# Kernel tuning notes

Hardware: AMD Instinct MI355X
Metric: run time of the kernel (lower is better)

The kernel has to match this reference:

```python
import jax, jax.numpy as jnp
import numpy as np

TEMPERATURE = 1.0
EPS = 1e-5
COS_EPS = 1e-8  # torch CosineSimilarity default eps
N_POS, N_NEG, D = 512, 512, 512


def setup_inputs() -> dict:
    key = jax.random.key(0)
    k1, k2, k3 = jax.random.split(key, 3)
    tensor_positive = jax.random.normal(k1, (N_POS, D), dtype=jnp.float32)
    tensor_negative = jax.random.normal(k2, (N_NEG, D), dtype=jnp.float32)
    # nn.Linear(512*3, 1), weight ~ N(0, 0.02^2), bias zeros
    linear_w = jax.random.normal(k3, (1, 3 * D), dtype=jnp.float32) * 0.02
    linear_b = jnp.zeros((1,), dtype=jnp.float32)
    return {"tensor_positive": tensor_positive, "tensor_negative": tensor_negative,
            "linear_w": linear_w, "linear_b": linear_b}


def _cos_matrix(a, b):
    # pairwise cosine similarity [Na, Nb], matching torch CosineSimilarity eps clamp
    an = a / jnp.maximum(jnp.linalg.norm(a, axis=-1, keepdims=True), COS_EPS)
    bn = b / jnp.maximum(jnp.linalg.norm(b, axis=-1, keepdims=True), COS_EPS)
    return an @ bn.T


def reference(tensor_positive, tensor_negative, linear_w, linear_b):
    pos, neg = tensor_positive, tensor_negative
    n_pos, d = pos.shape
    n_neg = neg.shape[0]

    # NCE part
    logit_n = jnp.exp(_cos_matrix(pos, neg) / TEMPERATURE)        # [N, M]
    deno_n = jnp.sum(logit_n, axis=-1)                            # [N]
    logit_p = jnp.exp(_cos_matrix(pos, pos) / TEMPERATURE)        # [N, N]
    loss = jnp.sum(-jnp.log(logit_p / (deno_n[:, None] + logit_p + EPS)))

    # Pairwise classifier: linear(cat([a, b, |a-b|])) decomposed as
    # a@w1 + b@w2 + |a-b|@w3 to avoid materializing the 3D concat.
    w = linear_w[0]
    w1, w2, w3 = w[:d], w[d:2 * d], w[2 * d:]
    allv = jnp.concatenate([pos, neg], axis=0)                    # [N+M, D]
    t1 = pos @ w1                                                 # [N]
    t2 = allv @ w2                                                # [N+M]
    diff = jnp.abs(pos[:, None, :] - allv[None, :, :])            # [N, N+M, D]
    t3 = jnp.einsum('nmd,d->nm', diff, w3)                        # [N, N+M]
    logits = t1[:, None] + t2[None, :] + t3 + linear_b[0]
    labels = jnp.concatenate([jnp.ones((n_pos,), jnp.float32),
                              jnp.zeros((n_neg,), jnp.float32)])  # [N+M]
    # BCE(sigmoid(logits), labels), stable form; per-i mean then sum over i
    bce = labels[None, :] * jax.nn.softplus(-logits) + (1.0 - labels[None, :]) * jax.nn.softplus(logits)
    loss = loss + jnp.sum(jnp.mean(bce, axis=1))
    return loss
```

## Files before the change

kernel.cpp:

```cpp
#include <hip/hip_runtime.h>
#include <math.h>

#define NPOS 512
#define DIM  512
#define NB   1024
#define EPSV 1e-5f
#define COS_EPS 1e-8f
#define ZSPLIT 4
#define KSLICE (DIM / ZSPLIT)

#define OFF_INV 0
#define OFF_T1  1024
#define OFF_T2  1536
#define OFF_P   2560
#define OFF_Q   (OFF_P + ZSPLIT * NPOS * NB)

__device__ __forceinline__ float softplus_f(float x) {
    return fmaxf(x, 0.f) + __logf(1.f + __expf(-fabsf(x)));
}

__global__ __launch_bounds__(256) void prep_kernel(
    const float* __restrict__ pos, const float* __restrict__ neg,
    const float* __restrict__ w, float* __restrict__ ws, float* __restrict__ out)
{
    int gtid = blockIdx.x * 256 + threadIdx.x;
    if (gtid == 0) out[0] = 0.f;
    int row  = gtid >> 6;
    int lane = threadIdx.x & 63;
    if (row >= NB) return;
    bool is_pos = row < NPOS;
    const float* r = is_pos ? pos + row * DIM : neg + (row - NPOS) * DIM;

    const float4* r4  = (const float4*)r + lane * 2;
    const float4* w14 = (const float4*)(w) + lane * 2;
    const float4* w24 = (const float4*)(w + DIM) + lane * 2;
    float4 a0 = r4[0],  a1 = r4[1];
    float4 u0 = w14[0], u1 = w14[1];
    float4 v0 = w24[0], v1 = w24[1];

    float ss  = a0.x*a0.x + a0.y*a0.y + a0.z*a0.z + a0.w*a0.w
              + a1.x*a1.x + a1.y*a1.y + a1.z*a1.z + a1.w*a1.w;
    float dw1 = a0.x*u0.x + a0.y*u0.y + a0.z*u0.z + a0.w*u0.w
              + a1.x*u1.x + a1.y*u1.y + a1.z*u1.z + a1.w*u1.w;
    float dw2 = a0.x*v0.x + a0.y*v0.y + a0.z*v0.z + a0.w*v0.w
              + a1.x*v1.x + a1.y*v1.y + a1.z*v1.z + a1.w*v1.w;

    #pragma unroll
    for (int off = 32; off; off >>= 1) {
        ss  += __shfl_xor(ss, off);
        dw1 += __shfl_xor(dw1, off);
        dw2 += __shfl_xor(dw2, off);
    }
    if (lane == 0) {
        float inv = 1.f / fmaxf(sqrtf(ss), COS_EPS);
        ws[OFF_INV + row] = inv;
        ws[OFF_T2 + row]  = dw2;
        if (is_pos) ws[OFF_T1 + row] = dw1;
    }
}

__global__ __launch_bounds__(256) void fused_kernel(
    const float* __restrict__ pos, const float* __restrict__ neg,
    const float* __restrict__ w, float* __restrict__ ws)
{
    __shared__ __align__(16) float As[64][36];
    __shared__ __align__(16) float Bs[64][36];

    const int tid = threadIdx.x;
    const int n0 = blockIdx.y * 64;
    const int m0 = blockIdx.x * 64;
    const int z  = blockIdx.z;
    const float* Asrc = pos + (size_t)n0 * DIM + z * KSLICE;
    const float* Bsrc = ((m0 < NPOS) ? (pos + (size_t)m0 * DIM)
                                     : (neg + (size_t)(m0 - NPOS) * DIM)) + z * KSLICE;
    const float* w3 = w + 2 * DIM + z * KSLICE;

    const int lr = tid >> 3;
    const int lc = (tid & 7) << 2;
    const int ti = tid >> 4;
    const int tj = tid & 15;

    float c[4][4] = {{0.f}}, t[4][4] = {{0.f}};

    float4 a0 = *(const float4*)(Asrc + lr * DIM + lc);
    float4 a1 = *(const float4*)(Asrc + (lr + 32) * DIM + lc);
    float4 b0 = *(const float4*)(Bsrc + lr * DIM + lc);
    float4 b1 = *(const float4*)(Bsrc + (lr + 32) * DIM + lc);
    *(float4*)&As[lr][lc]      = a0;
    *(float4*)&As[lr + 32][lc] = a1;
    *(float4*)&Bs[lr][lc]      = b0;
    *(float4*)&Bs[lr + 32][lc] = b1;
    __syncthreads();

    #pragma unroll 1
    for (int iter = 0; iter < KSLICE / 32; ++iter) {
        const bool more = (iter < KSLICE / 32 - 1);
        if (more) {
            const float* ap = Asrc + (iter + 1) * 32;
            const float* bp = Bsrc + (iter + 1) * 32;
            a0 = *(const float4*)(ap + lr * DIM + lc);
            a1 = *(const float4*)(ap + (lr + 32) * DIM + lc);
            b0 = *(const float4*)(bp + lr * DIM + lc);
            b1 = *(const float4*)(bp + (lr + 32) * DIM + lc);
        }
        const float* w3i = w3 + iter * 32;
        #pragma unroll
        for (int k = 0; k < 32; k += 4) {
            float4 av[4], bv[4];
            #pragma unroll
            for (int r = 0; r < 4; ++r) av[r] = *(const float4*)&As[ti + 16 * r][k];
            #pragma unroll
            for (int s = 0; s < 4; ++s) bv[s] = *(const float4*)&Bs[tj + 16 * s][k];
            const float4 wv = *(const float4*)(w3i + k);
            #pragma unroll
            for (int r = 0; r < 4; ++r) {
                #pragma unroll
                for (int s = 0; s < 4; ++s) {
                    c[r][s] = fmaf(av[r].x, bv[s].x, c[r][s]);
                    c[r][s] = fmaf(av[r].y, bv[s].y, c[r][s]);
                    c[r][s] = fmaf(av[r].z, bv[s].z, c[r][s]);
                    c[r][s] = fmaf(av[r].w, bv[s].w, c[r][s]);
                    t[r][s] = fmaf(fabsf(av[r].x - bv[s].x), wv.x, t[r][s]);
                    t[r][s] = fmaf(fabsf(av[r].y - bv[s].y), wv.y, t[r][s]);
                    t[r][s] = fmaf(fabsf(av[r].z - bv[s].z), wv.z, t[r][s]);
                    t[r][s] = fmaf(fabsf(av[r].w - bv[s].w), wv.w, t[r][s]);
                }
            }
        }
        if (more) {
            __syncthreads();
            *(float4*)&As[lr][lc]      = a0;
            *(float4*)&As[lr + 32][lc] = a1;
            *(float4*)&Bs[lr][lc]      = b0;
            *(float4*)&Bs[lr + 32][lc] = b1;
            __syncthreads();
        }
    }

    float* Sp = ws + OFF_P + (size_t)z * NPOS * NB;
    float* Tp = ws + OFF_Q + (size_t)z * NPOS * NB;
    #pragma unroll
    for (int r = 0; r < 4; ++r) {
        int n = n0 + ti + 16 * r;
        #pragma unroll
        for (int s = 0; s < 4; ++s) {
            int m = m0 + tj + 16 * s;
            Sp[(size_t)n * NB + m] = c[r][s];
            Tp[(size_t)n * NB + m] = t[r][s];
        }
    }
}

__global__ __launch_bounds__(128) void finish_kernel(
    const float* __restrict__ lb, float* __restrict__ ws, float* __restrict__ out)
{
    const int n = blockIdx.x * 2 + (threadIdx.x >> 6);
    const int l = threadIdx.x & 63;
    const float4* S[ZSPLIT];
    const float4* T[ZSPLIT];
    #pragma unroll
    for (int zz = 0; zz < ZSPLIT; ++zz) {
        S[zz] = (const float4*)(ws + OFF_P + (size_t)zz * NPOS * NB + (size_t)n * NB);
        T[zz] = (const float4*)(ws + OFF_Q + (size_t)zz * NPOS * NB + (size_t)n * NB);
    }
    const float invn = ws[OFF_INV + n];
    const float t1n  = ws[OFF_T1 + n];
    const float bias = lb[0];

    float4 cj[4];
    float eneg = 0.f;
    #pragma unroll
    for (int j = 0; j < 4; ++j) {
        int i4 = l + 64 * j;
        float4 s0 = S[0][i4], s1 = S[1][i4], s2 = S[2][i4], s3 = S[3][i4];
        float4 inv4 = *(const float4*)(ws + OFF_INV + 4 * i4);
        float4 cc;
        cc.x = (s0.x + s1.x + s2.x + s3.x) * invn * inv4.x;
        cc.y = (s0.y + s1.y + s2.y + s3.y) * invn * inv4.y;
        cc.z = (s0.z + s1.z + s2.z + s3.z) * invn * inv4.z;
        cc.w = (s0.w + s1.w + s2.w + s3.w) * invn * inv4.w;
        cj[j] = cc;
        if (j >= 2)
            eneg += __expf(cc.x) + __expf(cc.y) + __expf(cc.z) + __expf(cc.w);
    }
    #pragma unroll
    for (int off = 32; off; off >>= 1) eneg += __shfl_xor(eneg, off);

    float part = 0.f;
    #pragma unroll
    for (int j = 0; j < 2; ++j) {
        float4 cc = cj[j];
        part += __logf(eneg + __expf(cc.x) + EPSV) - cc.x;
        part += __logf(eneg + __expf(cc.y) + EPSV) - cc.y;
        part += __logf(eneg + __expf(cc.z) + EPSV) - cc.z;
        part += __logf(eneg + __expf(cc.w) + EPSV) - cc.w;
    }

    float bce = 0.f;
    #pragma unroll
    for (int j = 0; j < 4; ++j) {
        int i4 = l + 64 * j;
        float4 t0 = T[0][i4], t1 = T[1][i4], t2_ = T[2][i4], t3_ = T[3][i4];
        float4 tw = *(const float4*)(ws + OFF_T2 + 4 * i4);
        float4 lg;
        lg.x = t1n + tw.x + t0.x + t1.x + t2_.x + t3_.x + bias;
        lg.y = t1n + tw.y + t0.y + t1.y + t2_.y + t3_.y + bias;
        lg.z = t1n + tw.z + t0.z + t1.z + t2_.z + t3_.z + bias;
        lg.w = t1n + tw.w + t0.w + t1.w + t2_.w + t3_.w + bias;
        if (j < 2)
            bce += softplus_f(-lg.x) + softplus_f(-lg.y) + softplus_f(-lg.z) + softplus_f(-lg.w);
        else
            bce += softplus_f(lg.x) + softplus_f(lg.y) + softplus_f(lg.z) + softplus_f(lg.w);
    }
    part += bce * (1.f / 1024.f);

    #pragma unroll
    for (int off = 32; off; off >>= 1) part += __shfl_xor(part, off);
    if (l == 0) atomicAdd(out, part);
}

extern "C" void kernel_launch(void* const* d_in, const int* in_sizes, int n_in,
                              void* d_out, int out_size, void* d_ws, size_t ws_size,
                              hipStream_t stream) {
    (void)in_sizes; (void)n_in; (void)out_size; (void)ws_size;
    const float* pos = (const float*)d_in[0];
    const float* neg = (const float*)d_in[1];
    const float* w   = (const float*)d_in[2];
    const float* lb  = (const float*)d_in[3];
    float* out = (float*)d_out;
    float* ws  = (float*)d_ws;

    prep_kernel<<<256, 256, 0, stream>>>(pos, neg, w, ws, out);
    fused_kernel<<<dim3(16, 8, ZSPLIT), 256, 0, stream>>>(pos, neg, w, ws);
    finish_kernel<<<256, 128, 0, stream>>>(lb, ws, out);
}
```

Measured before the change: 109.9 us.

## Drop split-K partials and fuse BCE and negative row sums into main kernel epilogue

Removes the 4-way K split that wrote large partial S and T matrices to workspace. The fused kernel now loops over the full D dimension with 32x64 output tiles. Its epilogue computes the BCE softplus terms and the exp row sums over negatives directly, accumulating them with atomics. Only the positive-positive cosine block is stored for the finish kernel. This cuts tens of MB of workspace writes and reads. The cost is a longer per-block K loop, 256 blocks instead of 512, and per-element atomics for the denominators and the output.

Result: no change. 108.6 us (-1.1%).

```diff
diff --git a/kernel.cpp b/kernel.cpp
--- a/kernel.cpp
+++ b/kernel.cpp
@@ -6,14 +6,12 @@
 #define NB   1024
 #define EPSV 1e-5f
 #define COS_EPS 1e-8f
-#define ZSPLIT 4
-#define KSLICE (DIM / ZSPLIT)
-
-#define OFF_INV 0
-#define OFF_T1  1024
-#define OFF_T2  1536
-#define OFF_P   2560
-#define OFF_Q   (OFF_P + ZSPLIT * NPOS * NB)
+
+#define OFF_INV  0
+#define OFF_T1   1024
+#define OFF_T2   1536
+#define OFF_DENO 2560
+#define OFF_COS  3072
 
 __device__ __forceinline__ float softplus_f(float x) {
     return fmaxf(x, 0.f) + __logf(1.f + __expf(-fabsf(x)));
@@ -25,6 +23,7 @@
 {
     int gtid = blockIdx.x * 256 + threadIdx.x;
     if (gtid == 0) out[0] = 0.f;
+    if (gtid < NPOS) ws[OFF_DENO + gtid] = 0.f;
     int row  = gtid >> 6;
     int lane = threadIdx.x & 63;
     if (row >= NB) return;
@@ -61,59 +60,58 @@
 
 __global__ __launch_bounds__(256) void fused_kernel(
     const float* __restrict__ pos, const float* __restrict__ neg,
-    const float* __restrict__ w, float* __restrict__ ws)
+    const float* __restrict__ w, const float* __restrict__ lb,
+    float* __restrict__ ws, float* __restrict__ out)
 {
-    __shared__ __align__(16) float As[64][36];
+    __shared__ __align__(16) float As[32][36];
     __shared__ __align__(16) float Bs[64][36];
+    __shared__ float red[4];
 
     const int tid = threadIdx.x;
-    const int n0 = blockIdx.y * 64;
+    const int n0 = blockIdx.y * 32;
     const int m0 = blockIdx.x * 64;
-    const int z  = blockIdx.z;
-    const float* Asrc = pos + (size_t)n0 * DIM + z * KSLICE;
-    const float* Bsrc = ((m0 < NPOS) ? (pos + (size_t)m0 * DIM)
-                                     : (neg + (size_t)(m0 - NPOS) * DIM)) + z * KSLICE;
-    const float* w3 = w + 2 * DIM + z * KSLICE;
+    const bool isneg = (m0 >= NPOS);
+    const float* Asrc = pos + (size_t)n0 * DIM;
+    const float* Bsrc = isneg ? (neg + (size_t)(m0 - NPOS) * DIM)
+                              : (pos + (size_t)m0 * DIM);
+    const float* w3 = w + 2 * DIM;
 
     const int lr = tid >> 3;
     const int lc = (tid & 7) << 2;
     const int ti = tid >> 4;
     const int tj = tid & 15;
 
-    float c[4][4] = {{0.f}}, t[4][4] = {{0.f}};
+    float c[2][4] = {{0.f}}, t[2][4] = {{0.f}};
 
     float4 a0 = *(const float4*)(Asrc + lr * DIM + lc);
-    float4 a1 = *(const float4*)(Asrc + (lr + 32) * DIM + lc);
     float4 b0 = *(const float4*)(Bsrc + lr * DIM + lc);
     float4 b1 = *(const float4*)(Bsrc + (lr + 32) * DIM + lc);
     *(float4*)&As[lr][lc]      = a0;
-    *(float4*)&As[lr + 32][lc] = a1;
     *(float4*)&Bs[lr][lc]      = b0;
     *(float4*)&Bs[lr + 32][lc] = b1;
     __syncthreads();
 
     #pragma unroll 1
-    for (int iter = 0; iter < KSLICE / 32; ++iter) {
-        const bool more = (iter < KSLICE / 32 - 1);
+    for (int iter = 0; iter < DIM / 32; ++iter) {
+        const bool more = (iter < DIM / 32 - 1);
         if (more) {
             const float* ap = Asrc + (iter + 1) * 32;
             const float* bp = Bsrc + (iter + 1) * 32;
             a0 = *(const float4*)(ap + lr * DIM + lc);
-            a1 = *(const float4*)(ap + (lr + 32) * DIM + lc);
             b0 = *(const float4*)(bp + lr * DIM + lc);
             b1 = *(const float4*)(bp + (lr + 32) * DIM + lc);
         }
         const float* w3i = w3 + iter * 32;
         #pragma unroll
         for (int k = 0; k < 32; k += 4) {
-            float4 av[4], bv[4];
+            float4 av[2], bv[4];
             #pragma unroll
-            for (int r = 0; r < 4; ++r) av[r] = *(const float4*)&As[ti + 16 * r][k];
+            for (int r = 0; r < 2; ++r) av[r] = *(const float4*)&As[ti + 16 * r][k];
             #pragma unroll
             for (int s = 0; s < 4; ++s) bv[s] = *(const float4*)&Bs[tj + 16 * s][k];
             const float4 wv = *(const float4*)(w3i + k);
             #pragma unroll
-            for (int r = 0; r < 4; ++r) {
+            for (int r = 0; r < 2; ++r) {
                 #pragma unroll
                 for (int s = 0; s < 4; ++s) {
                     c[r][s] = fmaf(av[r].x, bv[s].x, c[r][s]);
@@ -130,89 +128,84 @@
         if (more) {
             __syncthreads();
             *(float4*)&As[lr][lc]      = a0;
-            *(float4*)&As[lr + 32][lc] = a1;
             *(float4*)&Bs[lr][lc]      = b0;
             *(float4*)&Bs[lr + 32][lc] = b1;
             __syncthreads();
         }
     }
 
-    float* Sp = ws + OFF_P + (size_t)z * NPOS * NB;
-    float* Tp = ws + OFF_Q + (size_t)z * NPOS * NB;
-    #pragma unroll
-    for (int r = 0; r < 4; ++r) {
+    const float bias = lb[0];
+    float inv_n[2], t1_n[2], inv_m[4], t2_m[4];
+    #pragma unroll
+    for (int r = 0; r < 2; ++r) {
         int n = n0 + ti + 16 * r;
+        inv_n[r] = ws[OFF_INV + n];
+        t1_n[r]  = ws[OFF_T1 + n];
+    }
+    #pragma unroll
+    for (int s = 0; s < 4; ++s) {
+        int m = m0 + tj + 16 * s;
+        inv_m[s] = ws[OFF_INV + m];
+        t2_m[s]  = ws[OFF_T2 + m];
+    }
+
+    float bce = 0.f;
+    float rowsum[2] = {0.f, 0.f};
+    #pragma unroll
+    for (int r = 0; r < 2; ++r) {
         #pragma unroll
         for (int s = 0; s < 4; ++s) {
-            int m = m0 + tj + 16 * s;
-            Sp[(size_t)n * NB + m] = c[r][s];
-            Tp[(size_t)n * NB + m] = t[r][s];
-        }
-    }
+            float cc = c[r][s] * inv_n[r] * inv_m[s];
+            float lg = t1_n[r] + t2_m[s] + t[r][s] + bias;
+            bce += softplus_f(isneg ? lg : -lg);
+            if (isneg) {
+                rowsum[r] += __expf(cc);
+            } else {
+                int n = n0 + ti + 16 * r;
+                int m = m0 + tj + 16 * s;
+                ws[OFF_COS + (size_t)n * NPOS + m] = cc;
+            }
+        }
+    }
+
+    if (isneg) {
+        #pragma unroll
+        for (int off = 1; off < 16; off <<= 1) {
+            rowsum[0] += __shfl_xor(rowsum[0], off);
+            rowsum[1] += __shfl_xor(rowsum[1], off);
+        }
+        if (tj == 0) {
+            atomicAdd(&ws[OFF_DENO + n0 + ti], rowsum[0]);
+            atomicAdd(&ws[OFF_DENO + n0 + ti + 16], rowsum[1]);
+        }
+    }
+
+    #pragma unroll
+    for (int off = 32; off; off >>= 1) bce += __shfl_xor(bce, off);
+    const int lane = tid & 63, wid = tid >> 6;
+    if (lane == 0) red[wid] = bce;
+    __syncthreads();
+    if (tid == 0)
+        atomicAdd(out, (red[0] + red[1] + red[2] + red[3]) * (1.f / 1024.f));
 }
 
 __global__ __launch_bounds__(128) void finish_kernel(
-    const float* __restrict__ lb, float* __restrict__ ws, float* __restrict__ out)
+    float* __restrict__ ws, float* __restrict__ out)
 {
     const int n = blockIdx.x * 2 + (threadIdx.x >> 6);
     const int l = threadIdx.x & 63;
-    const float4* S[ZSPLIT];
-    const float4* T[ZSPLIT];
-    #pragma unroll
-    for (int zz = 0; zz < ZSPLIT; ++zz) {
-        S[zz] = (const float4*)(ws + OFF_P + (size_t)zz * NPOS * NB + (size_t)n * NB);
-        T[zz] = (const float4*)(ws + OFF_Q + (size_t)zz * NPOS * NB + (size_t)n * NB);
-    }
-    const float invn = ws[OFF_INV + n];
-    const float t1n  = ws[OFF_T1 + n];
-    const float bias = lb[0];
-
-    float4 cj[4];
-    float eneg = 0.f;
-    #pragma unroll
-    for (int j = 0; j < 4; ++j) {
-        int i4 = l + 64 * j;
-        float4 s0 = S[0][i4], s1 = S[1][i4], s2 = S[2][i4], s3 = S[3][i4];
-        float4 inv4 = *(const float4*)(ws + OFF_INV + 4 * i4);
-        float4 cc;
-        cc.x = (s0.x + s1.x + s2.x + s3.x) * invn * inv4.x;
-        cc.y = (s0.y + s1.y + s2.y + s3.y) * invn * inv4.y;
-        cc.z = (s0.z + s1.z + s2.z + s3.z) * invn * inv4.z;
-        cc.w = (s0.w + s1.w + s2.w + s3.w) * invn * inv4.w;
-        cj[j] = cc;
-        if (j >= 2)
-            eneg += __expf(cc.x) + __expf(cc.y) + __expf(cc.z) + __expf(cc.w);
-    }
-    #pragma unroll
-    for (int off = 32; off; off >>= 1) eneg += __shfl_xor(eneg, off);
+    const float4* C = (const float4*)(ws + OFF_COS + (size_t)n * NPOS);
+    const float deno = ws[OFF_DENO + n];
 
     float part = 0.f;
     #pragma unroll
     for (int j = 0; j < 2; ++j) {
-        float4 cc = cj[j];
-        part += __logf(eneg + __expf(cc.x) + EPSV) - cc.x;
-        part += __logf(eneg + __expf(cc.y) + EPSV) - cc.y;
-        part += __logf(eneg + __expf(cc.z) + EPSV) - cc.z;
-        part += __logf(eneg + __expf(cc.w) + EPSV) - cc.w;
-    }
-
-    float bce = 0.f;
-    #pragma unroll
-    for (int j = 0; j < 4; ++j) {
-        int i4 = l + 64 * j;
-        float4 t0 = T[0][i4], t1 = T[1][i4], t2_ = T[2][i4], t3_ = T[3][i4];
-        float4 tw = *(const float4*)(ws + OFF_T2 + 4 * i4);
-        float4 lg;
-        lg.x = t1n + tw.x + t0.x + t1.x + t2_.x + t3_.x + bias;
-        lg.y = t1n + tw.y + t0.y + t1.y + t2_.y + t3_.y + bias;
-        lg.z = t1n + tw.z + t0.z + t1.z + t2_.z + t3_.z + bias;
-        lg.w = t1n + tw.w + t0.w + t1.w + t2_.w + t3_.w + bias;
-        if (j < 2)
-            bce += softplus_f(-lg.x) + softplus_f(-lg.y) + softplus_f(-lg.z) + softplus_f(-lg.w);
-        else
-            bce += softplus_f(lg.x) + softplus_f(lg.y) + softplus_f(lg.z) + softplus_f(lg.w);
-    }
-    part += bce * (1.f / 1024.f);
+        float4 cc = C[l + 64 * j];
+        part += __logf(deno + __expf(cc.x) + EPSV) - cc.x;
+        part += __logf(deno + __expf(cc.y) + EPSV) - cc.y;
+        part += __logf(deno + __expf(cc.z) + EPSV) - cc.z;
+        part += __logf(deno + __expf(cc.w) + EPSV) - cc.w;
+    }
 
     #pragma unroll
     for (int off = 32; off; off >>= 1) part += __shfl_xor(part, off);
@@ -231,6 +224,6 @@
     float* ws  = (float*)d_ws;
 
     prep_kernel<<<256, 256, 0, stream>>>(pos, neg, w, ws, out);
-    fused_kernel<<<dim3(16, 8, ZSPLIT), 256, 0, stream>>>(pos, neg, w, ws);
-    finish_kernel<<<256, 128, 0, stream>>>(lb, ws, out);
-}
+    fused_kernel<<<dim3(16, 16), 256, 0, stream>>>(pos, neg, w, lb, ws, out);
+    finish_kernel<<<256, 128, 0, stream>>>(ws, out);
+}
```
